# Optimization experiments

Hardware: AMD Instinct MI355X
Metric: run time of the kernel (lower is better)

The kernel has to match this reference:

```python
import jax, jax.numpy as jnp
import numpy as np
import math

BLKQ = 64
BLKK = 32
TOPK_FRAC = 0.1


def setup_inputs() -> dict:
    key = jax.random.key(0)
    k1, k2, k3, k4, k5 = jax.random.split(key, 5)
    B, L, H, D = 1, 8192, 16, 64
    q = jax.random.normal(k1, (B, L, H, D), jnp.float32)
    k = jax.random.normal(k2, (B, L, H, D), jnp.float32)
    v = jax.random.normal(k3, (B, L, H, D), jnp.float32)
    # proj_l initialized with nn.init.normal_ (std=1) in the original
    W_proj = jax.random.normal(k4, (D, D), jnp.float32)
    b_proj = jax.random.normal(k5, (D,), jnp.float32)
    return {"q": q, "k": k, "v": v, "W_proj": W_proj, "b_proj": b_proj}


def reference(q, k, v, W_proj, b_proj):
    B, L, H, D = q.shape
    lcm = BLKQ * BLKK // math.gcd(BLKQ, BLKK)
    L_pad = ((L + lcm - 1) // lcm) * lcm
    pad = L_pad - L
    scale = 1.0 / math.sqrt(D)

    # [B, L, H, D] -> [B, H, L_pad, D], zero padded (fused_transpose_pad)
    qt = jnp.transpose(q, (0, 2, 1, 3))
    kt = jnp.transpose(k, (0, 2, 1, 3))
    vt = jnp.transpose(v, (0, 2, 1, 3))
    if pad:
        pw = ((0, 0), (0, 0), (0, pad), (0, 0))
        qt_p = jnp.pad(qt, pw); kt_p = jnp.pad(kt, pw); vt_p = jnp.pad(vt, pw)
    else:
        qt_p, kt_p, vt_p = qt, kt, vt

    # key smoothing (SAGE): subtract per-(b,h) mean of padded k
    km = kt_p.mean(axis=-2, keepdims=True)          # [B, H, 1, D]
    kc = kt_p - km

    M = L_pad // BLKQ
    N = L_pad // BLKK
    # block pooling for routing scores
    pooled_q = qt_p.reshape(B, H, M, BLKQ, D).mean(axis=3)   # [B,H,M,D]
    pooled_k = kc.reshape(B, H, N, BLKK, D).mean(axis=3)     # [B,H,N,D]
    score = jnp.einsum('bhmd,bhnd->bhmn', pooled_q, pooled_k)

    T = min(N, int(TOPK_FRAC * N))                  # real_topk (static)
    _, idx = jax.lax.top_k(score, T)                # [B,H,M,T]
    lut = jnp.sort(idx, axis=-1)

    # gather selected key/value blocks: [B,H,M,T,BLKK,D]
    kb = kc.reshape(B, H, N, BLKK, D)
    vb = vt_p.reshape(B, H, N, BLKK, D)
    kg = jnp.take_along_axis(kb[:, :, None], lut[..., None, None], axis=3)
    vg = jnp.take_along_axis(vb[:, :, None], lut[..., None, None], axis=3)

    qb = qt_p.reshape(B, H, M, BLKQ, D)
    # block-sparse scores: [B,H,M,BLKQ,T,BLKK]
    s = jnp.einsum('bhmqd,bhmtkd->bhmqtk', qb, kg) * scale
    key_pos = lut[..., None] * BLKK + jnp.arange(BLKK)       # [B,H,M,T,BLKK]
    valid = key_pos < L
    s = jnp.where(valid[:, :, :, None, :, :], s, -jnp.inf)
    s = s.reshape(B, H, M, BLKQ, T * BLKK)
    p = jax.nn.softmax(s, axis=-1)
    o_s = jnp.einsum('bhmqn,bhmnd->bhmqd', p, vg.reshape(B, H, M, T * BLKK, D))
    o_s = o_s.reshape(B, H, L_pad, D)[:, :, :L]              # slice to seq_len

    # linear attention branch (softmax feature map over D)
    q_fm = jax.nn.softmax(qt_p[:, :, :L], axis=-1)
    k_fm = jax.nn.softmax(kt_p[:, :, :L], axis=-1)
    kvsum = jnp.einsum('bhld,bhle->bhde', k_fm, vt)          # [B,H,D,D]
    ksum = k_fm.sum(axis=-2)                                 # [B,H,D]
    denom = jnp.einsum('bhld,bhd->bhl', q_fm, ksum)[..., None] + 1e-6
    o_l = jnp.einsum('bhld,bhde->bhle', q_fm, kvsum) / denom
    o_l = o_l @ W_proj.T + b_proj                            # proj_l

    o = jnp.transpose(o_l + o_s, (0, 2, 1, 3))               # [B,L,H,D]
    return o
```

## Files before the change

kernel.cpp:

```cpp
#include <hip/hip_runtime.h>
#include <math.h>

#define SEQL 8192
#define NH 16
#define HD 1024
#define TSEL 25

#define OFF_KVPART 0
#define OFF_KSUM   262144
#define OFF_ZEND   263168
#define OFF_PK     263168
#define OFF_KWT    525312
#define OFF_KSWZ   558080
#define OFF_LUT    131072

typedef __attribute__((ext_vector_type(8))) short bf16x8;
typedef __attribute__((ext_vector_type(4))) float f32x4;

static __device__ inline short f2bf(float f) {
    union { float f; unsigned u; } c; c.f = f;
    unsigned r = (c.u + 0x7FFFu + ((c.u >> 16) & 1u)) >> 16;
    return (short)r;
}
static __device__ inline bf16x8 cvt8(float4 a, float4 b) {
    bf16x8 r;
    r[0] = f2bf(a.x); r[1] = f2bf(a.y); r[2] = f2bf(a.z); r[3] = f2bf(a.w);
    r[4] = f2bf(b.x); r[5] = f2bf(b.y); r[6] = f2bf(b.z); r[7] = f2bf(b.w);
    return r;
}
static __device__ inline unsigned cvtpk(float a, float b) {
    unsigned r;
    asm("v_cvt_pk_bf16_f32 %0, %1, %2" : "=v"(r) : "v"(a), "v"(b));
    return r;
}
static __device__ inline float exp2a(float x) {
#if __has_builtin(__builtin_amdgcn_exp2f)
    return __builtin_amdgcn_exp2f(x);
#else
    float r; asm("v_exp_f32 %0, %1" : "=v"(r) : "v"(x)); return r;
#endif
}
static __device__ inline void load_lds16(const void* g, void* l) {
    __builtin_amdgcn_global_load_lds((const __attribute__((address_space(1))) unsigned int*)g,
                                     (__attribute__((address_space(3))) unsigned int*)l,
                                     16, 0, 0);
}

__global__ __launch_bounds__(256) void prep_kv(const float* __restrict__ k,
                                               const float* __restrict__ v,
                                               short* __restrict__ kswz,
                                               short* __restrict__ vswz,
                                               float* __restrict__ pk) {
    __shared__ float pcol[4][64];
    int b = blockIdx.x;
    int h = b >> 8, n = b & 255;
    int t = threadIdx.x;
    {
        int r = t >> 3, ch = t & 7;
        const float* src = k + (size_t)(n * 32 + r) * HD + h * 64 + ch * 8;
        float4 f0 = *(const float4*)src, f1 = *(const float4*)(src + 4);
        int f = r * 8 + (ch ^ (r & 7));
        *(bf16x8*)(kswz + (size_t)b * 2048 + f * 8) = cvt8(f0, f1);
        float s[8] = { f0.x, f0.y, f0.z, f0.w, f1.x, f1.y, f1.z, f1.w };
        #pragma unroll
        for (int j = 0; j < 8; j++) {
            s[j] += __shfl_xor(s[j], 8, 64);
            s[j] += __shfl_xor(s[j], 16, 64);
            s[j] += __shfl_xor(s[j], 32, 64);
        }
        if ((t & 63) < 8) {
            #pragma unroll
            for (int j = 0; j < 8; j++) pcol[t >> 6][(t & 7) * 8 + j] = s[j];
        }
    }
    {
        int c = t >> 6, d = t & 63;
        const float* src = v + (size_t)(n * 32 + c * 8) * HD + h * 64 + d;
        bf16x8 val;
        #pragma unroll
        for (int j = 0; j < 8; j++) val[j] = f2bf(src[(size_t)j * HD]);
        int f = d * 4 + (c ^ ((d >> 1) & 3));
        *(bf16x8*)(vswz + (size_t)b * 2048 + f * 8) = val;
    }
    __syncthreads();
    if (t < 64)
        pk[(size_t)b * 64 + t] =
            (pcol[0][t] + pcol[1][t] + pcol[2][t] + pcol[3][t]) * (1.f / 32.f);
}

__global__ __launch_bounds__(256) void score_topk(const float* __restrict__ q,
                                                  const float* __restrict__ pk,
                                                  int* __restrict__ lut) {
    __shared__ __align__(16) float pq_s[64];
    __shared__ __align__(16) float s_s[256];
    __shared__ int wcnt[4];
    int b = blockIdx.x;
    int h = b >> 7, m = b & 127;
    int t = threadIdx.x;
    int lane = t & 63, w = t >> 6;
    if (t < 64) {
        const float* base = q + (size_t)m * 64 * HD + h * 64 + t;
        float s = 0.f;
        #pragma unroll 8
        for (int r = 0; r < 64; r++) s += base[(size_t)r * HD];
        pq_s[t] = s * (1.f / 64.f);
    }
    __syncthreads();
    const float* kr = pk + ((size_t)h * 256 + t) * 64;
    double acc = 0.0;
    #pragma unroll 8
    for (int d = 0; d < 64; d++) acc += (double)pq_s[d] * (double)kr[d];
    float sc = (float)acc;
    s_s[t] = sc;
    __syncthreads();
    int cnt = 0;
    float si = sc;
    #pragma unroll 4
    for (int j4 = 0; j4 < 64; j4++) {
        float4 sv = *(const float4*)&s_s[j4 * 4];
        int j = j4 * 4;
        cnt += (sv.x > si) || (sv.x == si && (j + 0) < t);
        cnt += (sv.y > si) || (sv.y == si && (j + 1) < t);
        cnt += (sv.z > si) || (sv.z == si && (j + 2) < t);
        cnt += (sv.w > si) || (sv.w == si && (j + 3) < t);
    }
    bool sel = cnt < TSEL;
    unsigned long long bal = __ballot(sel);
    if (lane == 0) wcnt[w] = __popcll(bal);
    __syncthreads();
    if (sel) {
        int off = __popcll(bal & ((1ull << lane) - 1ull));
        for (int i = 0; i < w; i++) off += wcnt[i];
        lut[(size_t)b * TSEL + off] = t;
    }
}

__global__ __launch_bounds__(256) void lin_kv(const float* __restrict__ k,
                                              const float* __restrict__ v,
                                              float* __restrict__ kvpart,
                                              float* __restrict__ ksum) {
    __shared__ __align__(16) float kf[2][64][68];
    __shared__ __align__(16) float vv[2][64][68];
    int b = blockIdx.x;
    int h = b >> 5, sc = b & 31;
    int l0 = sc * 256;
    int t = threadIdx.x;
    int lane = t & 63, w = t >> 6;
    int row = t >> 2, c16 = (t & 3) * 16;
    int d0 = (lane >> 4) * 4 + w * 16;
    int e0 = (lane & 15) * 4;
    float acc[16];
    #pragma unroll
    for (int i = 0; i < 16; i++) acc[i] = 0.f;
    float ks_acc = 0.f;

    const float* kbase = k + (size_t)(l0 + row) * HD + h * 64 + c16;
    const float* vbase = v + (size_t)(l0 + row) * HD + h * 64 + c16;
    float4 X0 = *(const float4*)(kbase);
    float4 X1 = *(const float4*)(kbase + 4);
    float4 X2 = *(const float4*)(kbase + 8);
    float4 X3 = *(const float4*)(kbase + 12);
    float4 V0 = *(const float4*)(vbase);
    float4 V1 = *(const float4*)(vbase + 4);
    float4 V2 = *(const float4*)(vbase + 8);
    float4 V3 = *(const float4*)(vbase + 12);

    #pragma unroll
    for (int ph = 0; ph < 4; ph++) {
        int buf = ph & 1;
        {
            float4* vd = (float4*)&vv[buf][row][c16];
            vd[0] = V0; vd[1] = V1; vd[2] = V2; vd[3] = V3;
        }
        float mx = fmaxf(fmaxf(fmaxf(X0.x, X0.y), fmaxf(X0.z, X0.w)),
                         fmaxf(fmaxf(X1.x, X1.y), fmaxf(X1.z, X1.w)));
        mx = fmaxf(mx, fmaxf(fmaxf(fmaxf(X2.x, X2.y), fmaxf(X2.z, X2.w)),
                             fmaxf(fmaxf(X3.x, X3.y), fmaxf(X3.z, X3.w))));
        mx = fmaxf(mx, __shfl_xor(mx, 1, 64));
        mx = fmaxf(mx, __shfl_xor(mx, 2, 64));
        X0.x = __expf(X0.x - mx); X0.y = __expf(X0.y - mx); X0.z = __expf(X0.z - mx); X0.w = __expf(X0.w - mx);
        X1.x = __expf(X1.x - mx); X1.y = __expf(X1.y - mx); X1.z = __expf(X1.z - mx); X1.w = __expf(X1.w - mx);
        X2.x = __expf(X2.x - mx); X2.y = __expf(X2.y - mx); X2.z = __expf(X2.z - mx); X2.w = __expf(X2.w - mx);
        X3.x = __expf(X3.x - mx); X3.y = __expf(X3.y - mx); X3.z = __expf(X3.z - mx); X3.w = __expf(X3.w - mx);
        float sm = (X0.x + X0.y + X0.z + X0.w) + (X1.x + X1.y + X1.z + X1.w)
                 + (X2.x + X2.y + X2.z + X2.w) + (X3.x + X3.y + X3.z + X3.w);
        sm += __shfl_xor(sm, 1, 64);
        sm += __shfl_xor(sm, 2, 64);
        float inv = 1.f / sm;
        X0.x *= inv; X0.y *= inv; X0.z *= inv; X0.w *= inv;
        X1.x *= inv; X1.y *= inv; X1.z *= inv; X1.w *= inv;
        X2.x *= inv; X2.y *= inv; X2.z *= inv; X2.w *= inv;
        X3.x *= inv; X3.y *= inv; X3.z *= inv; X3.w *= inv;
        {
            float4* kd = (float4*)&kf[buf][row][c16];
            kd[0] = X0; kd[1] = X1; kd[2] = X2; kd[3] = X3;
        }
        if (ph < 3) {
            const float* kn = kbase + (size_t)(ph + 1) * 64 * HD;
            const float* vn = vbase + (size_t)(ph + 1) * 64 * HD;
            X0 = *(const float4*)(kn);     X1 = *(const float4*)(kn + 4);
            X2 = *(const float4*)(kn + 8); X3 = *(const float4*)(kn + 12);
            V0 = *(const float4*)(vn);     V1 = *(const float4*)(vn + 4);
            V2 = *(const float4*)(vn + 8); V3 = *(const float4*)(vn + 12);
        }
        __syncthreads();
        #pragma unroll 8
        for (int l = 0; l < 64; l++) {
            float4 kd = *(const float4*)&kf[buf][l][d0];
            float4 ve = *(const float4*)&vv[buf][l][e0];
            acc[0]  += kd.x * ve.x; acc[1]  += kd.x * ve.y; acc[2]  += kd.x * ve.z; acc[3]  += kd.x * ve.w;
            acc[4]  += kd.y * ve.x; acc[5]  += kd.y * ve.y; acc[6]  += kd.y * ve.z; acc[7]  += kd.y * ve.w;
            acc[8]  += kd.z * ve.x; acc[9]  += kd.z * ve.y; acc[10] += kd.z * ve.z; acc[11] += kd.z * ve.w;
            acc[12] += kd.w * ve.x; acc[13] += kd.w * ve.y; acc[14] += kd.w * ve.z; acc[15] += kd.w * ve.w;
        }
        if (t < 64) {
            float s = 0.f;
            #pragma unroll 8
            for (int l = 0; l < 64; l++) s += kf[buf][l][t];
            ks_acc += s;
        }
    }
    float* dst = kvpart + ((size_t)(sc & 3) * 16 + h) * 4096;
    #pragma unroll
    for (int i = 0; i < 4; i++)
        #pragma unroll
        for (int j = 0; j < 4; j++)
            atomicAdd(&dst[(d0 + i) * 64 + e0 + j], acc[i * 4 + j]);
    if (t < 64) atomicAdd(&ksum[h * 64 + t], ks_acc);
}

__global__ __launch_bounds__(256) void kw_mul(const float* __restrict__ kvpart,
                                              const float* __restrict__ W,
                                              short* __restrict__ kwt) {
    __shared__ __align__(16) float kv[16][68];
    __shared__ __align__(16) float wsm[64][68];
    int h = blockIdx.x >> 2, dq = blockIdx.x & 3;
    int t = threadIdx.x;
    for (int i = t; i < 1024; i += 256) {
        int dl = i >> 6, e = i & 63;
        float s = 0.f;
        #pragma unroll
        for (int p = 0; p < 4; p++)
            s += kvpart[((size_t)p * 16 + h) * 4096 + (dq * 16 + dl) * 64 + e];
        kv[dl][e] = s;
    }
    for (int i = t; i < 4096; i += 256) wsm[i >> 6][i & 63] = W[i];
    __syncthreads();
    int lane = t & 63, wi = t >> 6;
    int dl = lane & 15;
    int db = wi * 16 + (lane >> 4) * 4;
    #pragma unroll
    for (int j = 0; j < 4; j++) {
        int dd = db + j;
        float a = 0.f;
        #pragma unroll
        for (int e4 = 0; e4 < 16; e4++) {
            float4 kq = *(const float4*)&kv[dl][e4 * 4];
            float4 wq = *(const float4*)&wsm[dd][e4 * 4];
            a += kq.x * wq.x + kq.y * wq.y + kq.z * wq.z + kq.w * wq.w;
        }
        kwt[(size_t)h * 4096 + dd * 64 + dq * 16 + dl] = f2bf(a);
    }
}

__global__ __launch_bounds__(256) void sparse_attn_mfma(const float* __restrict__ q,
                                                        const short* __restrict__ kswz,
                                                        const short* __restrict__ vswz,
                                                        const int* __restrict__ lut,
                                                        const short* __restrict__ kwt,
                                                        const float* __restrict__ ksum,
                                                        const float* __restrict__ bproj,
                                                        float* __restrict__ out) {
    __shared__ __align__(16) short Kb[2][2048];
    __shared__ __align__(16) short Vb[2][2048];
    __shared__ __align__(16) short Pl[64][40];
    __shared__ int lut_s[TSEL];

    int b = blockIdx.x;
    int x = b & 7, jj = b >> 3;
    int h = x * 2 + (jj >> 7);
    int m = jj & 127;
    int t = threadIdx.x;
    int lane = t & 63, w = t >> 6;
    int l15 = lane & 15, quad = lane >> 4;

    if (t < TSEL) lut_s[t] = lut[(size_t)(h * 128 + m) * TSEL + t];
    __syncthreads();

    {
        size_t base = (size_t)(h * 256 + lut_s[0]) * 2048;
        load_lds16(kswz + base + t * 8, &Kb[0][t * 8]);
        load_lds16(vswz + base + t * 8, &Vb[0][t * 8]);
        load_lds16(kwt + (size_t)h * 4096 + t * 8, &Kb[1][t * 8]);
        load_lds16(kwt + (size_t)h * 4096 + 2048 + t * 8, &Vb[1][t * 8]);
    }

    const float* qrow = q + (size_t)(m * 64 + w * 16 + l15) * HD + h * 64;
    float4 x0 = *(const float4*)(qrow + quad * 8);
    float4 x1 = *(const float4*)(qrow + quad * 8 + 4);
    float4 x2 = *(const float4*)(qrow + 32 + quad * 8);
    float4 x3 = *(const float4*)(qrow + 32 + quad * 8 + 4);
    bf16x8 qa[2];
    qa[0] = cvt8(x0, x1);
    qa[1] = cvt8(x2, x3);

    float mx = fmaxf(fmaxf(fmaxf(x0.x, x0.y), fmaxf(x0.z, x0.w)),
                     fmaxf(fmaxf(x1.x, x1.y), fmaxf(x1.z, x1.w)));
    mx = fmaxf(mx, fmaxf(fmaxf(fmaxf(x2.x, x2.y), fmaxf(x2.z, x2.w)),
                         fmaxf(fmaxf(x3.x, x3.y), fmaxf(x3.z, x3.w))));
    mx = fmaxf(mx, __shfl_xor(mx, 16, 64));
    mx = fmaxf(mx, __shfl_xor(mx, 32, 64));
    x0.x = __expf(x0.x - mx); x0.y = __expf(x0.y - mx); x0.z = __expf(x0.z - mx); x0.w = __expf(x0.w - mx);
    x1.x = __expf(x1.x - mx); x1.y = __expf(x1.y - mx); x1.z = __expf(x1.z - mx); x1.w = __expf(x1.w - mx);
    x2.x = __expf(x2.x - mx); x2.y = __expf(x2.y - mx); x2.z = __expf(x2.z - mx); x2.w = __expf(x2.w - mx);
    x3.x = __expf(x3.x - mx); x3.y = __expf(x3.y - mx); x3.z = __expf(x3.z - mx); x3.w = __expf(x3.w - mx);
    float sm = (x0.x + x0.y + x0.z + x0.w) + (x1.x + x1.y + x1.z + x1.w)
             + (x2.x + x2.y + x2.z + x2.w) + (x3.x + x3.y + x3.z + x3.w);
    sm += __shfl_xor(sm, 16, 64);
    sm += __shfl_xor(sm, 32, 64);
    float qsc = 1.f / sm;
    float4 ka0 = *(const float4*)(ksum + h * 64 + quad * 8);
    float4 ka1 = *(const float4*)(ksum + h * 64 + quad * 8 + 4);
    float4 ka2 = *(const float4*)(ksum + h * 64 + 32 + quad * 8);
    float4 ka3 = *(const float4*)(ksum + h * 64 + 32 + quad * 8 + 4);
    float dq = x0.x * ka0.x + x0.y * ka0.y + x0.z * ka0.z + x0.w * ka0.w
             + x1.x * ka1.x + x1.y * ka1.y + x1.z * ka1.z + x1.w * ka1.w
             + x2.x * ka2.x + x2.y * ka2.y + x2.z * ka2.z + x2.w * ka2.w
             + x3.x * ka3.x + x3.y * ka3.y + x3.z * ka3.z + x3.w * ka3.w;
    dq += __shfl_xor(dq, 16, 64);
    dq += __shfl_xor(dq, 32, 64);
    float invd = 1.f / (dq * qsc + 1e-6f);
    x0.x *= qsc; x0.y *= qsc; x0.z *= qsc; x0.w *= qsc;
    x1.x *= qsc; x1.y *= qsc; x1.z *= qsc; x1.w *= qsc;
    x2.x *= qsc; x2.y *= qsc; x2.z *= qsc; x2.w *= qsc;
    x3.x *= qsc; x3.y *= qsc; x3.z *= qsc; x3.w *= qsc;
    bf16x8 qf[2];
    qf[0] = cvt8(x0, x1);
    qf[1] = cvt8(x2, x3);

    __syncthreads();

    f32x4 Ol[4];
    #pragma unroll
    for (int dt = 0; dt < 4; dt++) Ol[dt] = (f32x4){0.f, 0.f, 0.f, 0.f};
    __builtin_amdgcn_s_setprio(1);
    #pragma unroll
    for (int dt = 0; dt < 4; dt++) {
        #pragma unroll
        for (int kc = 0; kc < 2; kc++) {
            int flat = (dt * 16 + l15) * 64 + kc * 32 + quad * 8;
            bf16x8 a = (dt < 2) ? *(const bf16x8*)&Kb[1][flat]
                                : *(const bf16x8*)&Vb[1][flat - 2048];
            Ol[dt] = __builtin_amdgcn_mfma_f32_16x16x32_bf16(a, qf[kc], Ol[dt], 0, 0, 0);
        }
    }
    __builtin_amdgcn_s_setprio(0);

    f32x4 O[4];
    #pragma unroll
    for (int dt = 0; dt < 4; dt++) O[dt] = (f32x4){0.f, 0.f, 0.f, 0.f};
    float l_i = 0.f;
    const f32x4 z = (f32x4){0.f, 0.f, 0.f, 0.f};
    const float EC = 1.44269504f * 0.125f;

    for (int ti = 0; ti < TSEL; ti++) {
        __syncthreads();
        int buf = ti & 1;
        if (ti + 1 < TSEL) {
            size_t base = (size_t)(h * 256 + lut_s[ti + 1]) * 2048;
            load_lds16(kswz + base + t * 8, &Kb[buf ^ 1][t * 8]);
            load_lds16(vswz + base + t * 8, &Vb[buf ^ 1][t * 8]);
        }
        int r0 = l15, r1 = 16 + l15;
        bf16x8 a00 = *(const bf16x8*)&Kb[buf][(r0 * 8 + (quad ^ (r0 & 7))) * 8];
        bf16x8 a01 = *(const bf16x8*)&Kb[buf][(r0 * 8 + ((4 + quad) ^ (r0 & 7))) * 8];
        bf16x8 a10 = *(const bf16x8*)&Kb[buf][(r1 * 8 + (quad ^ (r1 & 7))) * 8];
        bf16x8 a11 = *(const bf16x8*)&Kb[buf][(r1 * 8 + ((4 + quad) ^ (r1 & 7))) * 8];
        __builtin_amdgcn_s_setprio(1);
        f32x4 s0 = __builtin_amdgcn_mfma_f32_16x16x32_bf16(a00, qa[0], z, 0, 0, 0);
        s0 = __builtin_amdgcn_mfma_f32_16x16x32_bf16(a01, qa[1], s0, 0, 0, 0);
        f32x4 s1 = __builtin_amdgcn_mfma_f32_16x16x32_bf16(a10, qa[0], z, 0, 0, 0);
        s1 = __builtin_amdgcn_mfma_f32_16x16x32_bf16(a11, qa[1], s1, 0, 0, 0);
        __builtin_amdgcn_s_setprio(0);

        float p0[4], p1[4];
        float lsum = 0.f;
        #pragma unroll
        for (int r = 0; r < 4; r++) {
            p0[r] = exp2a(s0[r] * EC);
            p1[r] = exp2a(s1[r] * EC);
            lsum += p0[r] + p1[r];
        }
        lsum += __shfl_xor(lsum, 16, 64);
        lsum += __shfl_xor(lsum, 32, 64);
        l_i += lsum;

        uint2 pkA, pkB;
        pkA.x = cvtpk(p0[0], p0[1]); pkA.y = cvtpk(p0[2], p0[3]);
        pkB.x = cvtpk(p1[0], p1[1]); pkB.y = cvtpk(p1[2], p1[3]);
        *(uint2*)&Pl[w * 16 + l15][quad * 4] = pkA;
        *(uint2*)&Pl[w * 16 + l15][16 + quad * 4] = pkB;

        asm volatile("s_waitcnt lgkmcnt(0)\n\ts_barrier" ::: "memory");

        bf16x8 pb = *(const bf16x8*)&Pl[w * 16 + l15][quad * 8];
        __builtin_amdgcn_s_setprio(1);
        #pragma unroll
        for (int dt = 0; dt < 4; dt++) {
            int d = dt * 16 + l15;
            bf16x8 va = *(const bf16x8*)&Vb[buf][(d * 4 + (quad ^ ((d >> 1) & 3))) * 8];
            O[dt] = __builtin_amdgcn_mfma_f32_16x16x32_bf16(va, pb, O[dt], 0, 0, 0);
        }
        __builtin_amdgcn_s_setprio(0);
    }

    float inv = 1.f / l_i;
    float* dst = out + (size_t)(m * 64 + w * 16 + l15) * HD + h * 64;
    #pragma unroll
    for (int dt = 0; dt < 4; dt++) {
        float4 bv = *(const float4*)(bproj + dt * 16 + quad * 4);
        float4 o;
        o.x = O[dt][0] * inv + Ol[dt][0] * invd + bv.x;
        o.y = O[dt][1] * inv + Ol[dt][1] * invd + bv.y;
        o.z = O[dt][2] * inv + Ol[dt][2] * invd + bv.z;
        o.w = O[dt][3] * inv + Ol[dt][3] * invd + bv.w;
        *(float4*)(dst + dt * 16 + quad * 4) = o;
    }
}

extern "C" void kernel_launch(void* const* d_in, const int* in_sizes, int n_in,
                              void* d_out, int out_size, void* d_ws, size_t ws_size,
                              hipStream_t stream) {
    const float* q  = (const float*)d_in[0];
    const float* k  = (const float*)d_in[1];
    const float* v  = (const float*)d_in[2];
    const float* W  = (const float*)d_in[3];
    const float* bp = (const float*)d_in[4];
    float* out = (float*)d_out;
    float* ws = (float*)d_ws;

    float* kvpart = ws + OFF_KVPART;
    float* ksum   = ws + OFF_KSUM;
    float* pk     = ws + OFF_PK;
    short* kwt    = (short*)(ws + OFF_KWT);
    short* kswz   = (short*)(ws + OFF_KSWZ);
    short* vswz   = kswz + (size_t)16 * 256 * 2048;
    int*   lut    = (int*)(ws + OFF_LUT);

    hipMemsetAsync(ws, 0, OFF_ZEND * sizeof(float), stream);
    prep_kv<<<4096, 256, 0, stream>>>(k, v, kswz, vswz, pk);
    lin_kv<<<512, 256, 0, stream>>>(k, v, kvpart, ksum);
    kw_mul<<<64, 256, 0, stream>>>(kvpart, W, kwt);
    score_topk<<<2048, 256, 0, stream>>>(q, pk, lut);
    sparse_attn_mfma<<<2048, 256, 0, stream>>>(q, kswz, vswz, lut, kwt, ksum, bp, out);
}
```

Baseline: 286.0 us.

## Fuse K/V prep into linear-attention kernel and triple-buffer sparse attention loads

Merges prep_kv and lin_kv into one prep_lin kernel, so K and V are read from global memory once and the bf16 swizzled copies, pooled keys and linear-attention partial sums all come from the same registers and LDS tiles. This removes a full pass over K and V plus a kernel launch. The sparse attention loop moves from double to triple buffering with a prefetch distance of two and vmcnt-based waits, and the barrier after the P write is dropped. The fused kernel launches only 512 blocks where prep_kv had 4096, which lowers parallelism. Dropping the barrier relies on each wave reading only its own rows of Pl.

```diff
diff --git a/kernel.cpp b/kernel.cpp
--- a/kernel.cpp
+++ b/kernel.cpp
@@ -46,46 +46,173 @@
                                      16, 0, 0);
 }
 
-__global__ __launch_bounds__(256) void prep_kv(const float* __restrict__ k,
-                                               const float* __restrict__ v,
-                                               short* __restrict__ kswz,
-                                               short* __restrict__ vswz,
-                                               float* __restrict__ pk) {
-    __shared__ float pcol[4][64];
+__global__ __launch_bounds__(256) void prep_lin(const float* __restrict__ k,
+                                                const float* __restrict__ v,
+                                                short* __restrict__ kswz,
+                                                short* __restrict__ vswz,
+                                                float* __restrict__ pk,
+                                                float* __restrict__ kvpart,
+                                                float* __restrict__ ksum) {
+    __shared__ __align__(16) float kf[2][64][68];
+    __shared__ __align__(16) float vv[2][64][68];
+    __shared__ float pcol[2][2][4][64];
     int b = blockIdx.x;
-    int h = b >> 8, n = b & 255;
+    int h = b >> 5, sc = b & 31;
     int t = threadIdx.x;
-    {
-        int r = t >> 3, ch = t & 7;
-        const float* src = k + (size_t)(n * 32 + r) * HD + h * 64 + ch * 8;
-        float4 f0 = *(const float4*)src, f1 = *(const float4*)(src + 4);
-        int f = r * 8 + (ch ^ (r & 7));
-        *(bf16x8*)(kswz + (size_t)b * 2048 + f * 8) = cvt8(f0, f1);
-        float s[8] = { f0.x, f0.y, f0.z, f0.w, f1.x, f1.y, f1.z, f1.w };
+    int lane = t & 63, w = t >> 6;
+    int r32 = t >> 3, ch = t & 7;
+    int d0 = (lane >> 4) * 4 + w * 16;
+    int e0 = (lane & 15) * 4;
+    float acc[16];
+    #pragma unroll
+    for (int i = 0; i < 16; i++) acc[i] = 0.f;
+    float ks_acc = 0.f;
+
+    const float* kb_ = k + (size_t)(sc * 256 + r32) * HD + h * 64 + ch * 8;
+    const float* vb_ = v + (size_t)(sc * 256 + r32) * HD + h * 64 + ch * 8;
+    float4 K0a = *(const float4*)kb_;
+    float4 K0b = *(const float4*)(kb_ + 4);
+    float4 K1a = *(const float4*)(kb_ + (size_t)32 * HD);
+    float4 K1b = *(const float4*)(kb_ + (size_t)32 * HD + 4);
+    float4 V0a = *(const float4*)vb_;
+    float4 V0b = *(const float4*)(vb_ + 4);
+    float4 V1a = *(const float4*)(vb_ + (size_t)32 * HD);
+    float4 V1b = *(const float4*)(vb_ + (size_t)32 * HD + 4);
+
+    #pragma unroll
+    for (int ph = 0; ph < 4; ph++) {
+        int buf = ph & 1;
+        int n0 = sc * 8 + ph * 2;
+        {
+            *(float4*)&vv[buf][r32][ch * 8]          = V0a;
+            *(float4*)&vv[buf][r32][ch * 8 + 4]      = V0b;
+            *(float4*)&vv[buf][32 + r32][ch * 8]     = V1a;
+            *(float4*)&vv[buf][32 + r32][ch * 8 + 4] = V1b;
+        }
+        {
+            int f = r32 * 8 + (ch ^ (r32 & 7));
+            *(bf16x8*)(kswz + (size_t)(h * 256 + n0) * 2048 + f * 8)     = cvt8(K0a, K0b);
+            *(bf16x8*)(kswz + (size_t)(h * 256 + n0 + 1) * 2048 + f * 8) = cvt8(K1a, K1b);
+        }
+        {
+            float s_[8] = { K0a.x, K0a.y, K0a.z, K0a.w, K0b.x, K0b.y, K0b.z, K0b.w };
+            #pragma unroll
+            for (int j = 0; j < 8; j++) {
+                s_[j] += __shfl_xor(s_[j], 8, 64);
+                s_[j] += __shfl_xor(s_[j], 16, 64);
+                s_[j] += __shfl_xor(s_[j], 32, 64);
+            }
+            if (lane < 8) {
+                #pragma unroll
+                for (int j = 0; j < 8; j++) pcol[buf][0][w][(t & 7) * 8 + j] = s_[j];
+            }
+            float s1_[8] = { K1a.x, K1a.y, K1a.z, K1a.w, K1b.x, K1b.y, K1b.z, K1b.w };
+            #pragma unroll
+            for (int j = 0; j < 8; j++) {
+                s1_[j] += __shfl_xor(s1_[j], 8, 64);
+                s1_[j] += __shfl_xor(s1_[j], 16, 64);
+                s1_[j] += __shfl_xor(s1_[j], 32, 64);
+            }
+            if (lane < 8) {
+                #pragma unroll
+                for (int j = 0; j < 8; j++) pcol[buf][1][w][(t & 7) * 8 + j] = s1_[j];
+            }
+        }
+        {
+            float mx = fmaxf(fmaxf(fmaxf(K0a.x, K0a.y), fmaxf(K0a.z, K0a.w)),
+                             fmaxf(fmaxf(K0b.x, K0b.y), fmaxf(K0b.z, K0b.w)));
+            mx = fmaxf(mx, __shfl_xor(mx, 1, 64));
+            mx = fmaxf(mx, __shfl_xor(mx, 2, 64));
+            mx = fmaxf(mx, __shfl_xor(mx, 4, 64));
+            float4 Fa, Fb;
+            Fa.x = __expf(K0a.x - mx); Fa.y = __expf(K0a.y - mx);
+            Fa.z = __expf(K0a.z - mx); Fa.w = __expf(K0a.w - mx);
+            Fb.x = __expf(K0b.x - mx); Fb.y = __expf(K0b.y - mx);
+            Fb.z = __expf(K0b.z - mx); Fb.w = __expf(K0b.w - mx);
+            float sm = (Fa.x + Fa.y + Fa.z + Fa.w) + (Fb.x + Fb.y + Fb.z + Fb.w);
+            sm += __shfl_xor(sm, 1, 64);
+            sm += __shfl_xor(sm, 2, 64);
+            sm += __shfl_xor(sm, 4, 64);
+            float inv = 1.f / sm;
+            Fa.x *= inv; Fa.y *= inv; Fa.z *= inv; Fa.w *= inv;
+            Fb.x *= inv; Fb.y *= inv; Fb.z *= inv; Fb.w *= inv;
+            *(float4*)&kf[buf][r32][ch * 8]     = Fa;
+            *(float4*)&kf[buf][r32][ch * 8 + 4] = Fb;
+        }
+        {
+            float mx = fmaxf(fmaxf(fmaxf(K1a.x, K1a.y), fmaxf(K1a.z, K1a.w)),
+                             fmaxf(fmaxf(K1b.x, K1b.y), fmaxf(K1b.z, K1b.w)));
+            mx = fmaxf(mx, __shfl_xor(mx, 1, 64));
+            mx = fmaxf(mx, __shfl_xor(mx, 2, 64));
+            mx = fmaxf(mx, __shfl_xor(mx, 4, 64));
+            float4 Fa, Fb;
+            Fa.x = __expf(K1a.x - mx); Fa.y = __expf(K1a.y - mx);
+            Fa.z = __expf(K1a.z - mx); Fa.w = __expf(K1a.w - mx);
+            Fb.x = __expf(K1b.x - mx); Fb.y = __expf(K1b.y - mx);
+            Fb.z = __expf(K1b.z - mx); Fb.w = __expf(K1b.w - mx);
+            float sm = (Fa.x + Fa.y + Fa.z + Fa.w) + (Fb.x + Fb.y + Fb.z + Fb.w);
+            sm += __shfl_xor(sm, 1, 64);
+            sm += __shfl_xor(sm, 2, 64);
+            sm += __shfl_xor(sm, 4, 64);
+            float inv = 1.f / sm;
+            Fa.x *= inv; Fa.y *= inv; Fa.z *= inv; Fa.w *= inv;
+            Fb.x *= inv; Fb.y *= inv; Fb.z *= inv; Fb.w *= inv;
+            *(float4*)&kf[buf][32 + r32][ch * 8]     = Fa;
+            *(float4*)&kf[buf][32 + r32][ch * 8 + 4] = Fb;
+        }
+        if (ph < 3) {
+            const float* kn = kb_ + (size_t)(ph + 1) * 64 * HD;
+            const float* vn = vb_ + (size_t)(ph + 1) * 64 * HD;
+            K0a = *(const float4*)kn;
+            K0b = *(const float4*)(kn + 4);
+            K1a = *(const float4*)(kn + (size_t)32 * HD);
+            K1b = *(const float4*)(kn + (size_t)32 * HD + 4);
+            V0a = *(const float4*)vn;
+            V0b = *(const float4*)(vn + 4);
+            V1a = *(const float4*)(vn + (size_t)32 * HD);
+            V1b = *(const float4*)(vn + (size_t)32 * HD + 4);
+        }
+        __syncthreads();
+        if (t < 128) {
+            int s = t >> 6, d = t & 63;
+            pk[(size_t)(h * 256 + n0 + s) * 64 + d] =
+                (pcol[buf][s][0][d] + pcol[buf][s][1][d] + pcol[buf][s][2][d] + pcol[buf][s][3][d])
+                * (1.f / 32.f);
+        }
+        {
+            int c = w, d = lane;
+            #pragma unroll
+            for (int s = 0; s < 2; s++) {
+                bf16x8 val;
+                #pragma unroll
+                for (int j = 0; j < 8; j++) val[j] = f2bf(vv[buf][s * 32 + c * 8 + j][d]);
+                int f = d * 4 + (c ^ ((d >> 1) & 3));
+                *(bf16x8*)(vswz + (size_t)(h * 256 + n0 + s) * 2048 + f * 8) = val;
+            }
+        }
+        #pragma unroll 8
+        for (int l = 0; l < 64; l++) {
+            float4 kd = *(const float4*)&kf[buf][l][d0];
+            float4 ve = *(const float4*)&vv[buf][l][e0];
+            acc[0]  += kd.x * ve.x; acc[1]  += kd.x * ve.y; acc[2]  += kd.x * ve.z; acc[3]  += kd.x * ve.w;
+            acc[4]  += kd.y * ve.x; acc[5]  += kd.y * ve.y; acc[6]  += kd.y * ve.z; acc[7]  += kd.y * ve.w;
+            acc[8]  += kd.z * ve.x; acc[9]  += kd.z * ve.y; acc[10] += kd.z * ve.z; acc[11] += kd.z * ve.w;
+            acc[12] += kd.w * ve.x; acc[13] += kd.w * ve.y; acc[14] += kd.w * ve.z; acc[15] += kd.w * ve.w;
+        }
+        if (t < 64) {
+            float s = 0.f;
+            #pragma unroll 8
+            for (int l = 0; l < 64; l++) s += kf[buf][l][t];
+            ks_acc += s;
+        }
+    }
+    float* dst = kvpart + ((size_t)(sc & 3) * 16 + h) * 4096;
+    #pragma unroll
+    for (int i = 0; i < 4; i++)
         #pragma unroll
-        for (int j = 0; j < 8; j++) {
-            s[j] += __shfl_xor(s[j], 8, 64);
-            s[j] += __shfl_xor(s[j], 16, 64);
-            s[j] += __shfl_xor(s[j], 32, 64);
-        }
-        if ((t & 63) < 8) {
-            #pragma unroll
-            for (int j = 0; j < 8; j++) pcol[t >> 6][(t & 7) * 8 + j] = s[j];
-        }
-    }
-    {
-        int c = t >> 6, d = t & 63;
-        const float* src = v + (size_t)(n * 32 + c * 8) * HD + h * 64 + d;
-        bf16x8 val;
-        #pragma unroll
-        for (int j = 0; j < 8; j++) val[j] = f2bf(src[(size_t)j * HD]);
-        int f = d * 4 + (c ^ ((d >> 1) & 3));
-        *(bf16x8*)(vswz + (size_t)b * 2048 + f * 8) = val;
-    }
-    __syncthreads();
-    if (t < 64)
-        pk[(size_t)b * 64 + t] =
-            (pcol[0][t] + pcol[1][t] + pcol[2][t] + pcol[3][t]) * (1.f / 32.f);
+        for (int j = 0; j < 4; j++)
+            atomicAdd(&dst[(d0 + i) * 64 + e0 + j], acc[i * 4 + j]);
+    if (t < 64) atomicAdd(&ksum[h * 64 + t], ks_acc);
 }
 
 __global__ __launch_bounds__(256) void score_topk(const float* __restrict__ q,
@@ -135,100 +262,6 @@
     }
 }
 
-__global__ __launch_bounds__(256) void lin_kv(const float* __restrict__ k,
-                                              const float* __restrict__ v,
-                                              float* __restrict__ kvpart,
-                                              float* __restrict__ ksum) {
-    __shared__ __align__(16) float kf[2][64][68];
-    __shared__ __align__(16) float vv[2][64][68];
-    int b = blockIdx.x;
-    int h = b >> 5, sc = b & 31;
-    int l0 = sc * 256;
-    int t = threadIdx.x;
-    int lane = t & 63, w = t >> 6;
-    int row = t >> 2, c16 = (t & 3) * 16;
-    int d0 = (lane >> 4) * 4 + w * 16;
-    int e0 = (lane & 15) * 4;
-    float acc[16];
-    #pragma unroll
-    for (int i = 0; i < 16; i++) acc[i] = 0.f;
-    float ks_acc = 0.f;
-
-    const float* kbase = k + (size_t)(l0 + row) * HD + h * 64 + c16;
-    const float* vbase = v + (size_t)(l0 + row) * HD + h * 64 + c16;
-    float4 X0 = *(const float4*)(kbase);
-    float4 X1 = *(const float4*)(kbase + 4);
-    float4 X2 = *(const float4*)(kbase + 8);
-    float4 X3 = *(const float4*)(kbase + 12);
-    float4 V0 = *(const float4*)(vbase);
-    float4 V1 = *(const float4*)(vbase + 4);
-    float4 V2 = *(const float4*)(vbase + 8);
-    float4 V3 = *(const float4*)(vbase + 12);
-
-    #pragma unroll
-    for (int ph = 0; ph < 4; ph++) {
-        int buf = ph & 1;
-        {
-            float4* vd = (float4*)&vv[buf][row][c16];
-            vd[0] = V0; vd[1] = V1; vd[2] = V2; vd[3] = V3;
-        }
-        float mx = fmaxf(fmaxf(fmaxf(X0.x, X0.y), fmaxf(X0.z, X0.w)),
-                         fmaxf(fmaxf(X1.x, X1.y), fmaxf(X1.z, X1.w)));
-        mx = fmaxf(mx, fmaxf(fmaxf(fmaxf(X2.x, X2.y), fmaxf(X2.z, X2.w)),
-                             fmaxf(fmaxf(X3.x, X3.y), fmaxf(X3.z, X3.w))));
-        mx = fmaxf(mx, __shfl_xor(mx, 1, 64));
-        mx = fmaxf(mx, __shfl_xor(mx, 2, 64));
-        X0.x = __expf(X0.x - mx); X0.y = __expf(X0.y - mx); X0.z = __expf(X0.z - mx); X0.w = __expf(X0.w - mx);
-        X1.x = __expf(X1.x - mx); X1.y = __expf(X1.y - mx); X1.z = __expf(X1.z - mx); X1.w = __expf(X1.w - mx);
-        X2.x = __expf(X2.x - mx); X2.y = __expf(X2.y - mx); X2.z = __expf(X2.z - mx); X2.w = __expf(X2.w - mx);
-        X3.x = __expf(X3.x - mx); X3.y = __expf(X3.y - mx); X3.z = __expf(X3.z - mx); X3.w = __expf(X3.w - mx);
-        float sm = (X0.x + X0.y + X0.z + X0.w) + (X1.x + X1.y + X1.z + X1.w)
-                 + (X2.x + X2.y + X2.z + X2.w) + (X3.x + X3.y + X3.z + X3.w);
-        sm += __shfl_xor(sm, 1, 64);
-        sm += __shfl_xor(sm, 2, 64);
-        float inv = 1.f / sm;
-        X0.x *= inv; X0.y *= inv; X0.z *= inv; X0.w *= inv;
-        X1.x *= inv; X1.y *= inv; X1.z *= inv; X1.w *= inv;
-        X2.x *= inv; X2.y *= inv; X2.z *= inv; X2.w *= inv;
-        X3.x *= inv; X3.y *= inv; X3.z *= inv; X3.w *= inv;
-        {
-            float4* kd = (float4*)&kf[buf][row][c16];
-            kd[0] = X0; kd[1] = X1; kd[2] = X2; kd[3] = X3;
-        }
-        if (ph < 3) {
-            const float* kn = kbase + (size_t)(ph + 1) * 64 * HD;
-            const float* vn = vbase + (size_t)(ph + 1) * 64 * HD;
-            X0 = *(const float4*)(kn);     X1 = *(const float4*)(kn + 4);
-            X2 = *(const float4*)(kn + 8); X3 = *(const float4*)(kn + 12);
-            V0 = *(const float4*)(vn);     V1 = *(const float4*)(vn + 4);
-            V2 = *(const float4*)(vn + 8); V3 = *(const float4*)(vn + 12);
-        }
-        __syncthreads();
-        #pragma unroll 8
-        for (int l = 0; l < 64; l++) {
-            float4 kd = *(const float4*)&kf[buf][l][d0];
-            float4 ve = *(const float4*)&vv[buf][l][e0];
-            acc[0]  += kd.x * ve.x; acc[1]  += kd.x * ve.y; acc[2]  += kd.x * ve.z; acc[3]  += kd.x * ve.w;
-            acc[4]  += kd.y * ve.x; acc[5]  += kd.y * ve.y; acc[6]  += kd.y * ve.z; acc[7]  += kd.y * ve.w;
-            acc[8]  += kd.z * ve.x; acc[9]  += kd.z * ve.y; acc[10] += kd.z * ve.z; acc[11] += kd.z * ve.w;
-            acc[12] += kd.w * ve.x; acc[13] += kd.w * ve.y; acc[14] += kd.w * ve.z; acc[15] += kd.w * ve.w;
-        }
-        if (t < 64) {
-            float s = 0.f;
-            #pragma unroll 8
-            for (int l = 0; l < 64; l++) s += kf[buf][l][t];
-            ks_acc += s;
-        }
-    }
-    float* dst = kvpart + ((size_t)(sc & 3) * 16 + h) * 4096;
-    #pragma unroll
-    for (int i = 0; i < 4; i++)
-        #pragma unroll
-        for (int j = 0; j < 4; j++)
-            atomicAdd(&dst[(d0 + i) * 64 + e0 + j], acc[i * 4 + j]);
-    if (t < 64) atomicAdd(&ksum[h * 64 + t], ks_acc);
-}
-
 __global__ __launch_bounds__(256) void kw_mul(const float* __restrict__ kvpart,
                                               const float* __restrict__ W,
                                               short* __restrict__ kwt) {
@@ -271,9 +304,9 @@
                                                         const float* __restrict__ ksum,
                                                         const float* __restrict__ bproj,
                                                         float* __restrict__ out) {
-    __shared__ __align__(16) short Kb[2][2048];
-    __shared__ __align__(16) short Vb[2][2048];
-    __shared__ __align__(16) short Pl[64][40];
+    __shared__ __align__(16) short Kb[3][2048];
+    __shared__ __align__(16) short Vb[3][2048];
+    __shared__ __align__(16) short Pl[64][44];
     __shared__ int lut_s[TSEL];
 
     int b = blockIdx.x;
@@ -356,6 +389,13 @@
     }
     __builtin_amdgcn_s_setprio(0);
 
+    __syncthreads();
+    {
+        size_t base = (size_t)(h * 256 + lut_s[1]) * 2048;
+        load_lds16(kswz + base + t * 8, &Kb[1][t * 8]);
+        load_lds16(vswz + base + t * 8, &Vb[1][t * 8]);
+    }
+
     f32x4 O[4];
     #pragma unroll
     for (int dt = 0; dt < 4; dt++) O[dt] = (f32x4){0.f, 0.f, 0.f, 0.f};
@@ -363,19 +403,25 @@
     const f32x4 z = (f32x4){0.f, 0.f, 0.f, 0.f};
     const float EC = 1.44269504f * 0.125f;
 
+    int bc = 0;
     for (int ti = 0; ti < TSEL; ti++) {
-        __syncthreads();
-        int buf = ti & 1;
-        if (ti + 1 < TSEL) {
-            size_t base = (size_t)(h * 256 + lut_s[ti + 1]) * 2048;
-            load_lds16(kswz + base + t * 8, &Kb[buf ^ 1][t * 8]);
-            load_lds16(vswz + base + t * 8, &Vb[buf ^ 1][t * 8]);
+        if (ti > 0) {
+            if (ti < TSEL - 1) asm volatile("s_waitcnt vmcnt(2)" ::: "memory");
+            else               asm volatile("s_waitcnt vmcnt(0)" ::: "memory");
+            __builtin_amdgcn_s_barrier();
+            __builtin_amdgcn_sched_barrier(0);
+        }
+        if (ti + 2 < TSEL) {
+            int bs = bc ? bc - 1 : 2;
+            size_t base = (size_t)(h * 256 + lut_s[ti + 2]) * 2048;
+            load_lds16(kswz + base + t * 8, &Kb[bs][t * 8]);
+            load_lds16(vswz + base + t * 8, &Vb[bs][t * 8]);
         }
         int r0 = l15, r1 = 16 + l15;
-        bf16x8 a00 = *(const bf16x8*)&Kb[buf][(r0 * 8 + (quad ^ (r0 & 7))) * 8];
-        bf16x8 a01 = *(const bf16x8*)&Kb[buf][(r0 * 8 + ((4 + quad) ^ (r0 & 7))) * 8];
-        bf16x8 a10 = *(const bf16x8*)&Kb[buf][(r1 * 8 + (quad ^ (r1 & 7))) * 8];
-        bf16x8 a11 = *(const bf16x8*)&Kb[buf][(r1 * 8 + ((4 + quad) ^ (r1 & 7))) * 8];
+        bf16x8 a00 = *(const bf16x8*)&Kb[bc][(r0 * 8 + (quad ^ (r0 & 7))) * 8];
+        bf16x8 a01 = *(const bf16x8*)&Kb[bc][(r0 * 8 + ((4 + quad) ^ (r0 & 7))) * 8];
+        bf16x8 a10 = *(const bf16x8*)&Kb[bc][(r1 * 8 + (quad ^ (r1 & 7))) * 8];
+        bf16x8 a11 = *(const bf16x8*)&Kb[bc][(r1 * 8 + ((4 + quad) ^ (r1 & 7))) * 8];
         __builtin_amdgcn_s_setprio(1);
         f32x4 s0 = __builtin_amdgcn_mfma_f32_16x16x32_bf16(a00, qa[0], z, 0, 0, 0);
         s0 = __builtin_amdgcn_mfma_f32_16x16x32_bf16(a01, qa[1], s0, 0, 0, 0);
@@ -401,17 +447,20 @@
         *(uint2*)&Pl[w * 16 + l15][quad * 4] = pkA;
         *(uint2*)&Pl[w * 16 + l15][16 + quad * 4] = pkB;
 
-        asm volatile("s_waitcnt lgkmcnt(0)\n\ts_barrier" ::: "memory");
+        asm volatile("s_waitcnt lgkmcnt(0)" ::: "memory");
+        __builtin_amdgcn_sched_barrier(0);
 
         bf16x8 pb = *(const bf16x8*)&Pl[w * 16 + l15][quad * 8];
         __builtin_amdgcn_s_setprio(1);
         #pragma unroll
         for (int dt = 0; dt < 4; dt++) {
             int d = dt * 16 + l15;
-            bf16x8 va = *(const bf16x8*)&Vb[buf][(d * 4 + (quad ^ ((d >> 1) & 3))) * 8];
+            bf16x8 va = *(const bf16x8*)&Vb[bc][(d * 4 + (quad ^ ((d >> 1) & 3))) * 8];
             O[dt] = __builtin_amdgcn_mfma_f32_16x16x32_bf16(va, pb, O[dt], 0, 0, 0);
         }
         __builtin_amdgcn_s_setprio(0);
+
+        bc++; if (bc == 3) bc = 0;
     }
 
     float inv = 1.f / l_i;
@@ -448,8 +497,7 @@
     int*   lut    = (int*)(ws + OFF_LUT);
 
     hipMemsetAsync(ws, 0, OFF_ZEND * sizeof(float), stream);
-    prep_kv<<<4096, 256, 0, stream>>>(k, v, kswz, vswz, pk);
-    lin_kv<<<512, 256, 0, stream>>>(k, v, kvpart, ksum);
+    prep_lin<<<512, 256, 0, stream>>>(k, v, kswz, vswz, pk, kvpart, ksum);
     kw_mul<<<64, 256, 0, stream>>>(kvpart, W, kwt);
     score_topk<<<2048, 256, 0, stream>>>(q, pk, lut);
     sparse_attn_mfma<<<2048, 256, 0, stream>>>(q, kswz, vswz, lut, kwt, ksum, bp, out);
```

Result: faster. 267.9 us (-6.3%).
